# Performance work log

Hardware: AMD Instinct MI355X
Metric: run time of the kernel (lower is better)

## Reference

```python
import jax, jax.numpy as jnp
import numpy as np

B, C, N, V, W, D = 4, 64, 8, 32, 32, 256  # spa_dim = D


def _ln(x, g, b, eps=1e-5):
    m = jnp.mean(x, -1, keepdims=True)
    v = jnp.mean((x - m) ** 2, -1, keepdims=True)
    return (x - m) * jax.lax.rsqrt(v + eps) * g + b


def _tokens(x):
    # (b, c, n, v, w) -> (b*n, v*w, c)
    b, c, n, v, w = x.shape
    return x.transpose(0, 2, 3, 4, 1).reshape(b * n, v * w, c)


def setup_inputs() -> dict:
    key = jax.random.key(0)
    ks = jax.random.split(key, 8)
    fea_lf = jax.random.normal(ks[0], (B, C, N, V, W), jnp.float32)
    fea_hf = jax.random.normal(ks[1], (B, C, N, V, W), jnp.float32)
    W_in = jax.random.normal(ks[2], (C, D), jnp.float32) / np.sqrt(C)
    W_kv = jax.random.normal(ks[3], (C, 2 * D), jnp.float32) / np.sqrt(C)
    gamma = jnp.ones((D,), jnp.float32)
    beta = jnp.zeros((D,), jnp.float32)
    g2 = jnp.ones((D,), jnp.float32)
    b2 = jnp.zeros((D,), jnp.float32)
    W1 = jax.random.normal(ks[4], (D, 2 * D), jnp.float32) / np.sqrt(D)
    W2 = jax.random.normal(ks[5], (2 * D, D), jnp.float32) / np.sqrt(2 * D)
    W_out = jax.random.normal(ks[6], (D, C), jnp.float32) / np.sqrt(D)
    return {"fea_lf": fea_lf, "fea_hf": fea_hf, "W_in": W_in, "W_kv": W_kv,
            "gamma": gamma, "beta": beta, "g2": g2, "b2": b2,
            "W1": W1, "W2": W2, "W_out": W_out}


def reference(fea_lf, fea_hf, W_in, W_kv, gamma, beta, g2, b2, W1, W2, W_out):
    b, c, n, v, w = fea_lf.shape
    S = v * w
    tok_q = _tokens(fea_lf)   # (bn, S, c)
    tok_kv = _tokens(fea_hf)  # (bn, S, c)
    q = _ln(tok_q @ W_in, gamma, beta)              # (bn, S, D)
    kv = tok_kv @ W_kv
    k, vtok = jnp.split(kv, 2, axis=-1)
    k = _ln(k, gamma, beta)                          # shared LayerNorm (self.norm)
    # NOTE: original has no 1/sqrt(d) scaling on scores.
    score = jnp.einsum('bqd,bkd->bqk', q, k)         # (bn, S, S)
    mask = jnp.tril(jnp.ones((S, S), bool))
    score = jnp.where(mask, score, jnp.float32(-1e15))
    p = jax.nn.softmax(score, axis=-1)
    att = jnp.einsum('bqk,bkd->bqd', p, vtok)        # (bn, S, D)
    h = jax.nn.relu(_ln(att, g2, b2) @ W1) @ W2      # FFN (dropout=0)
    epi = h + vtok
    out = epi @ W_out                                # (bn, S, c)
    return out.reshape(b, n, v, w, c).transpose(0, 4, 1, 2, 3)
```

## Files before the change

kernel.cpp:

```cpp
#include <hip/hip_runtime.h>

typedef short bf16x8 __attribute__((ext_vector_type(8)));
typedef _Float16 f16x8 __attribute__((ext_vector_type(8)));
typedef float f32x4 __attribute__((ext_vector_type(4)));
typedef unsigned short u16;
typedef unsigned short u16x4 __attribute__((ext_vector_type(4)));

#define MFMA(a, b, c) __builtin_amdgcn_mfma_f32_16x16x32_bf16(a, b, c, 0, 0, 0)
#define MFMAH(a, b, c) __builtin_amdgcn_mfma_f32_16x16x32_f16(a, b, c, 0, 0, 0)

__device__ __forceinline__ u16 f2b(float f) {
    union { float f; unsigned u; } x{f};
    unsigned r = (x.u + 0x7FFFu + ((x.u >> 16) & 1u)) >> 16;
    return (u16)r;
}
__device__ __forceinline__ float b2f(u16 h) {
    union { unsigned u; float f; } x{((unsigned)h) << 16};
    return x.f;
}
__device__ __forceinline__ u16 f2h(float f) {
    _Float16 h = (_Float16)f;
    return *reinterpret_cast<u16*>(&h);
}
__device__ __forceinline__ float h2f(u16 h) {
    _Float16 v = *reinterpret_cast<_Float16*>(&h);
    return (float)v;
}
__device__ __forceinline__ float red16_sum(float v) {
#pragma unroll
    for (int m = 1; m < 16; m <<= 1) v += __shfl_xor(v, m, 64);
    return v;
}
__device__ __forceinline__ float red16_max(float v) {
#pragma unroll
    for (int m = 1; m < 16; m <<= 1) v = fmaxf(v, __shfl_xor(v, m, 64));
    return v;
}
__device__ __forceinline__ void gl_lds16(const void* g, void* l) {
    __builtin_amdgcn_global_load_lds(
        (const __attribute__((address_space(1))) unsigned int*)(g),
        (__attribute__((address_space(3))) unsigned int*)(l), 16, 0, 0);
}


__global__ __launch_bounds__(256) void wconv_kernel(
    const float* __restrict__ W1, const float* __restrict__ W2,
    const float* __restrict__ Wo, const float* __restrict__ Win,
    const float* __restrict__ Wkv, u16* __restrict__ w1T,
    u16* __restrict__ w2T, u16* __restrict__ woT, u16* __restrict__ wfrag) {
    int id = blockIdx.x * 256 + threadIdx.x;
    if (id < 131072) {
        int n = id >> 8, k = id & 255;
        w1T[id] = f2b(W1[k * 512 + n]);
    } else if (id < 262144) {
        int j = id - 131072;
        int n = j >> 9, k = j & 511;
        w2T[j] = f2b(W2[k * 256 + n]);
    } else if (id < 278528) {
        int j = id - 262144;
        int n = j >> 8, k = j & 255;
        woT[j] = f2b(Wo[k * 64 + n]);
    } else if (id < 284672) {
        int fid = id - 278528;
        int arr = fid >> 11;
        int e = fid & 2047;
        int ntck = e >> 6, ln = e & 63;
        int lr = ln & 15, lg2 = ln >> 4;
        int nt = ntck >> 1, ck = ntck & 1;
        int d = nt * 16 + lr;
#pragma unroll
        for (int j = 0; j < 8; j++) {
            int c = ck * 32 + lg2 * 8 + j;
            float x;
            if (arr == 0)      x = Win[c * 256 + d];
            else if (arr == 1) x = Wkv[c * 512 + d];
            else               x = Wkv[c * 512 + 256 + d];
            wfrag[arr * 16384 + e * 8 + j] = f2h(x);
        }
    }
}

#define PJ_A 0
#define PJ_WREG 16384
#define PJ_WORK 49152
__global__ __launch_bounds__(512, 1) void proj_kernel(
    const float* __restrict__ lf, const float* __restrict__ hf,
    const u16* __restrict__ wqg, const u16* __restrict__ wkg,
    const u16* __restrict__ wvg, const float* __restrict__ gamma,
    const float* __restrict__ beta, u16* __restrict__ qf_,
    u16* __restrict__ kf_, u16* __restrict__ vT) {
    extern __shared__ char sm[];
    const int tid = threadIdx.x;
    const int wave = tid >> 6, lane = tid & 63, lr = lane & 15, lg = lane >> 4;
    const int st = blockIdx.x, bn = blockIdx.y;
    const int b = bn >> 3, n = bn & 7;
    const int s0 = st * 128;
    const size_t baseF = (size_t)b * 524288 + (size_t)n * 1024 + s0;

    float gam[16], bet[16];
#pragma unroll
    for (int nt = 0; nt < 16; nt++) {
        gam[nt] = gamma[nt * 16 + lr];
        bet[nt] = beta[nt * 16 + lr];
    }

    auto stage32 = [&](const float* srcbase, int chalf) {
#pragma unroll
        for (int call = 0; call < 2; call++) {
            int unit = call * 8 + wave;
            int obase = unit << 10;
            int e = unit * 256 + lane * 4;
            int cl = e >> 7, si = e & 127;
            gl_lds16(srcbase + (size_t)(chalf * 32 + cl) * 8192 + si,
                     sm + PJ_WORK + obase);
        }
    };
    auto stageW = [&](const u16* wsrc) {
#pragma unroll
        for (int call = 0; call < 4; call++) {
            int obase = (call * 8 + wave) << 10;
            gl_lds16((const char*)wsrc + obase + lane * 16, sm + PJ_WREG + obase);
        }
    };
    auto buildA = [&](int slotbase) {
        int g = wave >> 1;
        int s = ((wave & 1) << 6) | lane;
        float x[8];
#pragma unroll
        for (int cc = 0; cc < 8; cc++)
            x[cc] = *(const float*)(sm + PJ_WORK + ((g * 8 + cc) << 9) + (s << 2));
        f16x8 ph;
#pragma unroll
        for (int cc = 0; cc < 8; cc++) ph[cc] = (_Float16)x[cc];
        int slp = (slotbase + g) ^ (s & 7);
        *(f16x8*)(sm + PJ_A + (s << 7) + (slp << 4)) = ph;
    };
    auto loadA = [&](f16x8* aF) {
        int tl = wave * 16 + lr;
#pragma unroll
        for (int ck = 0; ck < 2; ck++) {
            int off = (tl << 7) + ((((ck << 2) | lg) ^ (tl & 7)) << 4);
            aF[ck] = *(const f16x8*)(sm + PJ_A + off);
        }
    };
    auto pass1 = [&](const f16x8* aF, f32x4* acc) {
#pragma unroll
        for (int nt = 0; nt < 16; nt++) acc[nt] = (f32x4){0.f, 0.f, 0.f, 0.f};
#pragma unroll
        for (int nt = 0; nt < 16; nt++) {
#pragma unroll
            for (int ck = 0; ck < 2; ck++) {
                int wo = (((nt << 1) | ck) << 10) + (lane << 4);
                f16x8 bh = *(const f16x8*)(sm + PJ_WREG + wo);
                acc[nt] = MFMAH(aF[ck], bh, acc[nt]);
            }
        }
    };
    auto lnstats = [&](const f32x4* acc, float* mean, float* rs) {
#pragma unroll
        for (int r = 0; r < 4; r++) {
            float s1 = 0.f, s2 = 0.f;
#pragma unroll
            for (int nt = 0; nt < 16; nt++) {
                float xv = acc[nt][r];
                s1 += xv; s2 += xv * xv;
            }
            s1 = red16_sum(s1);
            s2 = red16_sum(s2);
            float mn = s1 * (1.f / 256.f);
            float var = s2 * (1.f / 256.f) - mn * mn;
            mean[r] = mn;
            rs[r] = rsqrtf(var + 1e-5f);
        }
    };
    auto emit = [&](const f32x4* acc, const float* mean, const float* rs,
                    u16* dst) {
        char* bw = sm + PJ_WORK + wave * 4096;
        const int gtok = bn * 1024 + s0 + wave * 16;
#pragma unroll
        for (int hh = 0; hh < 2; hh++) {
#pragma unroll
            for (int ntl = 0; ntl < 8; ntl++) {
                int nt = hh * 8 + ntl;
#pragma unroll
                for (int r = 0; r < 4; r++) {
                    float y = (acc[nt][r] - mean[r]) * rs[r] * gam[nt] + bet[nt];
                    int tl = lg * 4 + r;
                    int dl = ntl * 16 + lr;
                    int sl = dl >> 3;
                    *(u16*)(bw + tl * 256 + ((sl ^ ((tl >> 2) & 3)) << 4) +
                            (dl & 7) * 2) = f2h(y);
                }
            }
#pragma unroll
            for (int p = 0; p < 4; p++) {
                int row = lane >> 2, slq = (lane & 3) + p * 4;
                bf16x8 v8 = *(const bf16x8*)(bw + row * 256 +
                                             ((slq ^ ((row >> 2) & 3)) << 4));
                *(bf16x8*)(dst + (size_t)(gtok + row) * 256 + hh * 128 +
                           slq * 8) = v8;
            }
        }
    };

    f32x4 acc[16];
    float mean[4], rs[4];
    f16x8 aF[2];

    stage32(lf + baseF, 0);  __syncthreads();
    buildA(0);               __syncthreads();
    stage32(lf + baseF, 1);
    stageW(wqg);             __syncthreads();
    buildA(4);               __syncthreads();
    loadA(aF);
    pass1(aF, acc);
    lnstats(acc, mean, rs);  __syncthreads();
    stageW(wkg);
    emit(acc, mean, rs, qf_);
    __syncthreads();
    stage32(hf + baseF, 0);  __syncthreads();
    buildA(0);               __syncthreads();
    stage32(hf + baseF, 1);  __syncthreads();
    buildA(4);               __syncthreads();
    loadA(aF);
    pass1(aF, acc);
    lnstats(acc, mean, rs);  __syncthreads();
    stageW(wvg);
    emit(acc, mean, rs, kf_);
    __syncthreads();
    pass1(aF, acc);
#pragma unroll
    for (int nt = 0; nt < 16; nt++) {
        u16x4 pv;
#pragma unroll
        for (int r = 0; r < 4; r++) pv[r] = f2h(acc[nt][r]);
        *(u16x4*)(vT + ((size_t)(bn * 256) + nt * 16 + lr) * 1024 + s0 +
                  wave * 16 + lg * 4) = pv;
    }
}

__global__ __launch_bounds__(512) void attn_kernel(
    const u16* __restrict__ qf_, const u16* __restrict__ kf_,
    const u16* __restrict__ vT, const float* __restrict__ g2,
    const float* __restrict__ b2, u16* __restrict__ lnatt) {
    extern __shared__ char smem[];
    const int tid = threadIdx.x;
    const int wave = tid >> 6, lane = tid & 63, lr = lane & 15, lg = lane >> 4;
    const int grp = wave >> 2, w4 = wave & 3;
    const int b = blockIdx.x;
    const int bn = b & 31;
    const int strip = 15 - (b >> 5);
    const int qr0 = strip * 64 + w4 * 16;
    const int ni = strip + 1;
    const int ktbase = grp * ni;
    char* myK = smem + grp * 65536;
    char* myV = smem + grp * 65536 + 32768;
    u16* Pw = (u16*)(smem + 131072 + wave * 1280);

    f16x8 qf[8];
    {
        const size_t off = ((size_t)(bn * 1024 + qr0 + lr)) * 256 + lg * 8;
#pragma unroll
        for (int ck = 0; ck < 8; ck++)
            qf[ck] = *(const f16x8*)(qf_ + off + ck * 32);
    }
    f16x8 onesb;
    {
        _Float16 v1 = (lr == 0) ? (_Float16)1.0f : (_Float16)0.0f;
#pragma unroll
        for (int q = 0; q < 8; q++) onesb[q] = v1;
    }

    const int srl = lane >> 5, ss = lane & 31;
    const int vdl = lane >> 2, vg = lane & 3;
    auto stage = [&](int buf, int kt) {
        const int kv0 = kt << 5;
        char* baseK = myK + buf * 16384;
        char* baseV = myV + buf * 16384;
#pragma unroll
        for (int ii = 0; ii < 4; ii++) {
            int u = w4 * 4 + ii;
            int r = u * 2 + srl;
            size_t go = (((size_t)((bn << 10) + kv0 + r)) << 8) +
                        (unsigned)((ss ^ (r & 7)) << 3);
            gl_lds16(kf_ + go, baseK + u * 1024);
            int d = u * 16 + vdl;
            size_t gv = (((size_t)((bn << 8) + d)) << 10) + kv0 +
                        (unsigned)((vg ^ ((d >> 1) & 3)) << 3);
            gl_lds16(vT + gv, baseV + u * 1024);
        }
    };

    f32x4 o[16];
#pragma unroll
    for (int i = 0; i < 16; i++) o[i] = (f32x4){0.f, 0.f, 0.f, 0.f};
    f32x4 ol = (f32x4){0.f, 0.f, 0.f, 0.f};
    float m[4] = {-INFINITY, -INFINITY, -INFINITY, -INFINITY};

    stage(0, ktbase);
    for (int it = 0; it < ni; it++) {
        const int cur = it & 1;
        asm volatile("s_waitcnt vmcnt(0)" ::: "memory");
        __builtin_amdgcn_s_barrier();
        asm volatile("" ::: "memory");
        if (it + 1 < ni) stage(cur ^ 1, ktbase + it + 1);
        const int kt = ktbase + it;
        if ((kt << 5) <= qr0 + 15) {
            const char* kb = myK + cur * 16384;
            f32x4 sc0 = (f32x4){0.f, 0.f, 0.f, 0.f};
            f32x4 sc1 = (f32x4){0.f, 0.f, 0.f, 0.f};
            __builtin_amdgcn_s_setprio(1);
#pragma unroll
            for (int ck = 0; ck < 8; ck++) {
                int sw = ((ck * 4 + lg) ^ (lr & 7)) << 4;
                int a0 = lr * 512 + sw;
                f16x8 k0 = *(const f16x8*)(kb + a0);
                f16x8 k1 = *(const f16x8*)(kb + a0 + 8192);
                sc0 = MFMAH(qf[ck], k0, sc0);
                sc1 = MFMAH(qf[ck], k1, sc1);
            }
            __builtin_amdgcn_s_setprio(0);
            float scl[4];
            const int kvb = kt << 5;
#pragma unroll
            for (int r = 0; r < 4; r++) {
                int qi = qr0 + lg * 4 + r;
                float s0v = (kvb + lr > qi) ? -1e30f : sc0[r];
                float s1v = (kvb + 16 + lr > qi) ? -1e30f : sc1[r];
                float tm = red16_max(fmaxf(s0v, s1v));
                float mn = fmaxf(m[r], tm);
                scl[r] = __expf(m[r] - mn);
                m[r] = mn;
                int row = lg * 4 + r;
                Pw[row * 40 + lr] = f2h(__expf(s0v - mn));
                Pw[row * 40 + 16 + lr] = f2h(__expf(s1v - mn));
            }
#pragma unroll
            for (int f = 0; f < 16; f++) {
                f32x4 t = o[f];
                t[0] *= scl[0]; t[1] *= scl[1]; t[2] *= scl[2]; t[3] *= scl[3];
                o[f] = t;
            }
            ol[0] *= scl[0]; ol[1] *= scl[1]; ol[2] *= scl[2]; ol[3] *= scl[3];
            asm volatile("" ::: "memory");
            f16x8 pa = *(const f16x8*)((const char*)Pw + lr * 80 + lg * 16);
            const char* vb = myV + cur * 16384;
            __builtin_amdgcn_s_setprio(1);
#pragma unroll
            for (int db = 0; db < 16; db++) {
                int d = db * 16 + lr;
                f16x8 vf = *(const f16x8*)(vb + d * 64 +
                                           ((lg ^ ((lr >> 1) & 3)) << 4));
                o[db] = MFMAH(pa, vf, o[db]);
            }
            ol = MFMAH(pa, onesb, ol);
            __builtin_amdgcn_s_setprio(0);
        }
    }
    __syncthreads();
    float lsum[4];
#pragma unroll
    for (int r = 0; r < 4; r++) lsum[r] = __shfl(ol[r], lane & 48, 64);

    char* cb = smem + 65536;
    float* mlb = (float*)(smem + 131072);
    if (grp == 1) {
        char* po = cb + w4 * 16384;
#pragma unroll
        for (int f = 0; f < 16; f++)
            *(f32x4*)(po + (f * 16 + lr) * 64 + lg * 16) = o[f];
        if (lr == 0) {
#pragma unroll
            for (int r = 0; r < 4; r++) {
                int row = lg * 4 + r;
                mlb[(w4 * 16 + row) * 2] = m[r];
                mlb[(w4 * 16 + row) * 2 + 1] = lsum[r];
            }
        }
    }
    __syncthreads();
    if (grp == 0) {
        const char* po = cb + w4 * 16384;
        float e0[4], e1[4], linv[4];
#pragma unroll
        for (int r = 0; r < 4; r++) {
            int row = lg * 4 + r;
            float m1 = mlb[(w4 * 16 + row) * 2];
            float l1 = mlb[(w4 * 16 + row) * 2 + 1];
            float ms = fmaxf(m[r], m1);
            e0[r] = __expf(m[r] - ms);
            e1[r] = __expf(m1 - ms);
            linv[r] = 1.f / (lsum[r] * e0[r] + l1 * e1[r]);
        }
#pragma unroll
        for (int f = 0; f < 16; f++) {
            f32x4 o1 = *(const f32x4*)(po + (f * 16 + lr) * 64 + lg * 16);
#pragma unroll
            for (int r = 0; r < 4; r++)
                o[f][r] = (o[f][r] * e0[r] + o1[r] * e1[r]) * linv[r];
        }
        float gv[16], bv[16];
#pragma unroll
        for (int f = 0; f < 16; f++) {
            gv[f] = g2[f * 16 + lr];
            bv[f] = b2[f * 16 + lr];
        }
#pragma unroll
        for (int r = 0; r < 4; r++) {
            float s1 = 0.f, s2 = 0.f;
#pragma unroll
            for (int f = 0; f < 16; f++) {
                float x = o[f][r];
                s1 += x; s2 += x * x;
            }
            s1 = red16_sum(s1);
            s2 = red16_sum(s2);
            float mean = s1 * (1.f / 256.f);
            float var = s2 * (1.f / 256.f) - mean * mean;
            float rsv = rsqrtf(var + 1e-5f);
            size_t row = (size_t)(bn * 1024 + qr0 + lg * 4 + r) * 256;
#pragma unroll
            for (int f = 0; f < 16; f++)
                lnatt[row + f * 16 + lr] =
                    f2b((o[f][r] - mean) * rsv * gv[f] + bv[f]);
        }
    }
}

template <int K, int NB, int MODE>
__global__ __launch_bounds__(512) void gemmB_kernel(
    const u16* __restrict__ A, const u16* __restrict__ BT,
    u16* __restrict__ outb, const u16* __restrict__ vTr,
    float* __restrict__ outf, int ldOut) {
    extern __shared__ char bsm[];
    const int tid = threadIdx.x;
    const int wave = tid >> 6, lane = tid & 63, lr = lane & 15, lg = lane >> 4;
    constexpr int K2 = K * 2;
    constexpr int BN = NB * 16;
    constexpr int TILE = BN * K2;
    const int m0 = blockIdx.x * 128 + wave * 16;
    const int n0 = blockIdx.y * BN;
    {
        const char* bsrc = (const char*)(BT + (size_t)n0 * K);
        constexpr int ITER = TILE / (512 * 16);
#pragma unroll
        for (int it = 0; it < ITER; it++) {
            int o = (it * 512 + tid) * 16;
            int col = o / K2;
            int slot = (o % K2) >> 4;
            int src = col * K2 + ((slot ^ (col & 7)) << 4);
            gl_lds16(bsrc + src, bsm + o);
        }
    }
    __syncthreads();
    f32x4 acc[NB];
#pragma unroll
    for (int nb = 0; nb < NB; nb++) acc[nb] = (f32x4){0.f, 0.f, 0.f, 0.f};
    const u16* ap = A + (size_t)(m0 + lr) * K + lg * 8;
#pragma unroll
    for (int kc = 0; kc < K; kc += 32) {
        bf16x8 a = *(const bf16x8*)(ap + kc);
        int ks = (kc >> 3) + lg;
#pragma unroll
        for (int nb = 0; nb < NB; nb++) {
            int c = nb * 16 + lr;
            bf16x8 bv = *(const bf16x8*)(bsm + c * K2 + ((ks ^ (c & 7)) << 4));
            acc[nb] = MFMA(a, bv, acc[nb]);
        }
    }
    const int g = m0 + lg * 4;
    if (MODE == 0) {
#pragma unroll
        for (int nb = 0; nb < NB; nb++)
#pragma unroll
            for (int r = 0; r < 4; r++)
                outb[(size_t)(g + r) * ldOut + n0 + nb * 16 + lr] =
                    f2b(fmaxf(acc[nb][r], 0.f));
    } else if (MODE == 1) {
        int bn = g >> 10, s = g & 1023;
#pragma unroll
        for (int nb = 0; nb < NB; nb++) {
            int dd = n0 + nb * 16 + lr;
            u16x4 vv = *(const u16x4*)(vTr + ((size_t)bn * 256 + dd) * 1024 + s);
#pragma unroll
            for (int r = 0; r < 4; r++)
                outb[(size_t)(g + r) * 256 + dd] = f2b(acc[nb][r] + h2f(vv[r]));
        }
    } else {
        int bn = g >> 10, s = g & 1023;
        int bb = bn >> 3, nn = bn & 7;
#pragma unroll
        for (int nb = 0; nb < NB; nb++) {
            int cc = n0 + nb * 16 + lr;
            *(f32x4*)(outf + (size_t)bb * 524288 + (size_t)cc * 8192 +
                      (size_t)nn * 1024 + s) = acc[nb];
        }
    }
}

extern "C" void kernel_launch(void* const* d_in, const int* in_sizes, int n_in,
                              void* d_out, int out_size, void* d_ws, size_t ws_size,
                              hipStream_t stream) {
    const float* lf    = (const float*)d_in[0];
    const float* hf    = (const float*)d_in[1];
    const float* Win   = (const float*)d_in[2];
    const float* Wkv   = (const float*)d_in[3];
    const float* gamma = (const float*)d_in[4];
    const float* beta  = (const float*)d_in[5];
    const float* g2    = (const float*)d_in[6];
    const float* b2    = (const float*)d_in[7];
    const float* W1    = (const float*)d_in[8];
    const float* W2    = (const float*)d_in[9];
    const float* Wo    = (const float*)d_in[10];
    float* out = (float*)d_out;

    char* w = (char*)d_ws;
    const size_t MB16 = 16777216;
    u16* qf  = (u16*)(w);
    u16* kf  = (u16*)(w + MB16);
    u16* vT  = (u16*)(w + 2 * MB16);
    u16* hb  = (u16*)(w + 3 * MB16);
    u16* w1T = (u16*)(w + 3 * MB16 + 33554432);
    u16* w2T = w1T + 131072;
    u16* woT = w2T + 131072;
    u16* wfrag = woT + 16384;
    u16* wqg = wfrag;
    u16* wkg = wfrag + 16384;
    u16* wvg = wfrag + 32768;
    u16* lnatt = qf;
    u16* epib  = kf;

    wconv_kernel<<<dim3(1136), dim3(256), 0, stream>>>(W1, W2, Wo, Win, Wkv,
                                                       w1T, w2T, woT, wfrag);
    proj_kernel<<<dim3(8, 32), dim3(512), 81920, stream>>>(
        lf, hf, wqg, wkg, wvg, gamma, beta, qf, kf, vT);
    attn_kernel<<<dim3(512), dim3(512), 141312, stream>>>(qf, kf, vT, g2, b2,
                                                          lnatt);
    gemmB_kernel<256, 8, 0><<<dim3(256, 4), dim3(512), 65536, stream>>>(
        lnatt, w1T, hb, nullptr, nullptr, 512);
    gemmB_kernel<512, 8, 1><<<dim3(256, 2), dim3(512), 131072, stream>>>(
        hb, w2T, epib, vT, nullptr, 256);
    gemmB_kernel<256, 4, 2><<<dim3(256, 1), dim3(512), 32768, stream>>>(
        epib, woT, nullptr, nullptr, out, 64);
}
```

Measured before the change: 129.0 us.

## Single-buffer K/V tiles and fp16 partial output to cut attention LDS usage

The attention kernel drops double buffering of K/V tiles in shared memory and keeps one buffer per group, adding a second barrier per iteration before staging the next tile. The cross-group partial output exchange is stored as fp16 instead of fp32. Together these shrink dynamic LDS from about 138KB to about 74KB so two 512-thread blocks can fit per CU. The cost is that global-to-LDS loads no longer overlap compute within a block, and the partial accumulator loses precision.

Measured after the change: 135.6 us. 1.05x slower.

```diff
diff --git a/kernel.cpp b/kernel.cpp
--- a/kernel.cpp
+++ b/kernel.cpp
@@ -253,9 +253,9 @@
     const int qr0 = strip * 64 + w4 * 16;
     const int ni = strip + 1;
     const int ktbase = grp * ni;
-    char* myK = smem + grp * 65536;
-    char* myV = smem + grp * 65536 + 32768;
-    u16* Pw = (u16*)(smem + 131072 + wave * 1280);
+    char* myK = smem + grp * 32768;
+    char* myV = myK + 16384;
+    u16* Pw = (u16*)(smem + 65536 + wave * 1280);
 
     f16x8 qf[8];
     {
@@ -273,21 +273,19 @@
 
     const int srl = lane >> 5, ss = lane & 31;
     const int vdl = lane >> 2, vg = lane & 3;
-    auto stage = [&](int buf, int kt) {
+    auto stage = [&](int kt) {
         const int kv0 = kt << 5;
-        char* baseK = myK + buf * 16384;
-        char* baseV = myV + buf * 16384;
 #pragma unroll
         for (int ii = 0; ii < 4; ii++) {
             int u = w4 * 4 + ii;
             int r = u * 2 + srl;
             size_t go = (((size_t)((bn << 10) + kv0 + r)) << 8) +
                         (unsigned)((ss ^ (r & 7)) << 3);
-            gl_lds16(kf_ + go, baseK + u * 1024);
+            gl_lds16(kf_ + go, myK + u * 1024);
             int d = u * 16 + vdl;
             size_t gv = (((size_t)((bn << 8) + d)) << 10) + kv0 +
                         (unsigned)((vg ^ ((d >> 1) & 3)) << 3);
-            gl_lds16(vT + gv, baseV + u * 1024);
+            gl_lds16(vT + gv, myV + u * 1024);
         }
     };
 
@@ -297,16 +295,13 @@
     f32x4 ol = (f32x4){0.f, 0.f, 0.f, 0.f};
     float m[4] = {-INFINITY, -INFINITY, -INFINITY, -INFINITY};
 
-    stage(0, ktbase);
+    stage(ktbase);
     for (int it = 0; it < ni; it++) {
-        const int cur = it & 1;
         asm volatile("s_waitcnt vmcnt(0)" ::: "memory");
         __builtin_amdgcn_s_barrier();
         asm volatile("" ::: "memory");
-        if (it + 1 < ni) stage(cur ^ 1, ktbase + it + 1);
         const int kt = ktbase + it;
         if ((kt << 5) <= qr0 + 15) {
-            const char* kb = myK + cur * 16384;
             f32x4 sc0 = (f32x4){0.f, 0.f, 0.f, 0.f};
             f32x4 sc1 = (f32x4){0.f, 0.f, 0.f, 0.f};
             __builtin_amdgcn_s_setprio(1);
@@ -314,8 +309,8 @@
             for (int ck = 0; ck < 8; ck++) {
                 int sw = ((ck * 4 + lg) ^ (lr & 7)) << 4;
                 int a0 = lr * 512 + sw;
-                f16x8 k0 = *(const f16x8*)(kb + a0);
-                f16x8 k1 = *(const f16x8*)(kb + a0 + 8192);
+                f16x8 k0 = *(const f16x8*)(myK + a0);
+                f16x8 k1 = *(const f16x8*)(myK + a0 + 8192);
                 sc0 = MFMAH(qf[ck], k0, sc0);
                 sc1 = MFMAH(qf[ck], k1, sc1);
             }
@@ -344,31 +339,37 @@
             ol[0] *= scl[0]; ol[1] *= scl[1]; ol[2] *= scl[2]; ol[3] *= scl[3];
             asm volatile("" ::: "memory");
             f16x8 pa = *(const f16x8*)((const char*)Pw + lr * 80 + lg * 16);
-            const char* vb = myV + cur * 16384;
             __builtin_amdgcn_s_setprio(1);
 #pragma unroll
             for (int db = 0; db < 16; db++) {
                 int d = db * 16 + lr;
-                f16x8 vf = *(const f16x8*)(vb + d * 64 +
+                f16x8 vf = *(const f16x8*)(myV + d * 64 +
                                            ((lg ^ ((lr >> 1) & 3)) << 4));
                 o[db] = MFMAH(pa, vf, o[db]);
             }
             ol = MFMAH(pa, onesb, ol);
             __builtin_amdgcn_s_setprio(0);
         }
+        __builtin_amdgcn_s_barrier();
+        asm volatile("" ::: "memory");
+        if (it + 1 < ni) stage(ktbase + it + 1);
     }
     __syncthreads();
     float lsum[4];
 #pragma unroll
     for (int r = 0; r < 4; r++) lsum[r] = __shfl(ol[r], lane & 48, 64);
 
-    char* cb = smem + 65536;
-    float* mlb = (float*)(smem + 131072);
+    char* cb = smem + 32768;
+    float* mlb = (float*)(smem + 65536);
     if (grp == 1) {
-        char* po = cb + w4 * 16384;
-#pragma unroll
-        for (int f = 0; f < 16; f++)
-            *(f32x4*)(po + (f * 16 + lr) * 64 + lg * 16) = o[f];
+        char* po = cb + w4 * 8192;
+#pragma unroll
+        for (int f = 0; f < 16; f++) {
+            u16x4 ph;
+#pragma unroll
+            for (int r = 0; r < 4; r++) ph[r] = f2h(o[f][r]);
+            *(u16x4*)(po + (f * 16 + lr) * 32 + lg * 8) = ph;
+        }
         if (lr == 0) {
 #pragma unroll
             for (int r = 0; r < 4; r++) {
@@ -380,7 +381,7 @@
     }
     __syncthreads();
     if (grp == 0) {
-        const char* po = cb + w4 * 16384;
+        const char* po = cb + w4 * 8192;
         float e0[4], e1[4], linv[4];
 #pragma unroll
         for (int r = 0; r < 4; r++) {
@@ -394,10 +395,10 @@
         }
 #pragma unroll
         for (int f = 0; f < 16; f++) {
-            f32x4 o1 = *(const f32x4*)(po + (f * 16 + lr) * 64 + lg * 16);
+            u16x4 ph = *(const u16x4*)(po + (f * 16 + lr) * 32 + lg * 8);
 #pragma unroll
             for (int r = 0; r < 4; r++)
-                o[f][r] = (o[f][r] * e0[r] + o1[r] * e1[r]) * linv[r];
+                o[f][r] = (o[f][r] * e0[r] + h2f(ph[r]) * e1[r]) * linv[r];
         }
         float gv[16], bv[16];
 #pragma unroll
@@ -534,8 +535,8 @@
                                                        w1T, w2T, woT, wfrag);
     proj_kernel<<<dim3(8, 32), dim3(512), 81920, stream>>>(
         lf, hf, wqg, wkg, wvg, gamma, beta, qf, kf, vT);
-    attn_kernel<<<dim3(512), dim3(512), 141312, stream>>>(qf, kf, vT, g2, b2,
-                                                          lnatt);
+    attn_kernel<<<dim3(512), dim3(512), 75776, stream>>>(qf, kf, vT, g2, b2,
+                                                         lnatt);
     gemmB_kernel<256, 8, 0><<<dim3(256, 4), dim3(512), 65536, stream>>>(
         lnatt, w1T, hb, nullptr, nullptr, 512);
     gemmB_kernel<512, 8, 1><<<dim3(256, 2), dim3(512), 131072, stream>>>(
```
